# Optimization experiments

Hardware: AMD Instinct MI355X
Metric: run time of the kernel (lower is better)

## Reference

```python
import jax, jax.numpy as jnp
import numpy as np

N = 10000      # nodes
E = 160000     # edges
C = 128        # channels (hidden_irreps multiplicity)
NE = 10        # num_elements
G = 16         # num graphs
NB = 8         # num_bessel
RMAX = 5.0
PCUT = 5.0     # num_polynomial_cutoff
AVG_NN = 16.0
SQ3 = 3.0 ** 0.5


def _mlp(x, w1, w2, w3, wo):
    h = jax.nn.silu(x @ w1)
    h = jax.nn.silu(h @ w2)
    h = jax.nn.silu(h @ w3)
    return h @ wo


def _forward(positions, node_attrs, charges, shifts,
             W_emb, W_up1, Wr1_1, Wr1_2, Wr1_3, Wr1_o, Wlin1_s, Wlin1_v,
             P1_s1, P1_ss, P1_vv, P1_v1, P1_sv, Lp1_s, Lp1_v, R1,
             Wsk, Wup2_s, Wup2_v, Wr2_1, Wr2_2, Wr2_3, Wr2_o, Wlin2_s, Wlin2_v,
             P2_v1, P2_sv, Lp2_v, Rmid, Rout,
             edge_index, batch, num_graphs):
    snd, rcv = edge_index[0], edge_index[1]
    # edge vectors / lengths
    vec = positions[rcv] - positions[snd] + shifts                  # [E,3]
    length = jnp.sqrt(jnp.sum(vec * vec, -1) + 1e-12)               # [E]
    Yv = SQ3 * vec / length[:, None]                                # l=1 SH, component norm
    # Bessel radial basis * polynomial cutoff
    n = jnp.arange(1, NB + 1, dtype=positions.dtype)
    bess = (2.0 / RMAX) ** 0.5 * jnp.sin(n * jnp.pi * length[:, None] / RMAX) / length[:, None]
    u = length / RMAX
    p = PCUT
    fcut = jnp.where(u < 1.0,
                     1 - ((p + 1) * (p + 2) / 2) * u ** p + p * (p + 2) * u ** (p + 1)
                     - (p * (p + 1) / 2) * u ** (p + 2), 0.0)
    edge_feats = bess * fcut[:, None]                               # [E,NB]

    h = node_attrs @ W_emb                                          # node embedding [N,C]
    seg = lambda m: jax.ops.segment_sum(m, rcv, num_segments=N) / AVG_NN
    we = lambda Pm: node_attrs @ Pm                                 # element-dep. weights

    # ---- interaction / product / readout layer 1 (node feats are scalars) ----
    hu = h @ W_up1
    w = _mlp(edge_feats, Wr1_1, Wr1_2, Wr1_3, Wr1_o)                # [E,2C] TP weights
    w_ss, w_sv = w[:, :C], w[:, C:]
    hs_e = hu[snd]                                                  # gather sender feats
    A_s = seg(w_ss * hs_e)                                          # 0e x 0e -> 0e
    A_v = seg((w_sv * hs_e)[:, :, None] * Yv[:, None, :])           # 0e x 1o -> 1o
    A_s = A_s @ Wlin1_s
    A_v = jnp.einsum('ncd,ce->ned', A_v, Wlin1_v)
    # symmetric contraction (correlation=2), element-dependent weights
    B_s = we(P1_s1) * A_s + we(P1_ss) * A_s * A_s + we(P1_vv) * jnp.sum(A_v * A_v, -1) / SQ3
    B_v = we(P1_v1)[:, :, None] * A_v + we(P1_sv)[:, :, None] * A_s[:, :, None] * A_v
    h_s = B_s @ Lp1_s
    h_v = jnp.einsum('ncd,ce->ned', B_v, Lp1_v)
    dip1 = jnp.einsum('ncd,c->nd', h_v, R1)                         # linear dipole readout

    # ---- layer 2 (residual, output 128x1o) ----
    hs = h_s @ Wup2_s
    hv = jnp.einsum('ncd,ce->ned', h_v, Wup2_v)
    w2 = _mlp(edge_feats, Wr2_1, Wr2_2, Wr2_3, Wr2_o)               # [E,4C]
    w_a, w_b, w_c, w_d = w2[:, :C], w2[:, C:2 * C], w2[:, 2 * C:3 * C], w2[:, 3 * C:]
    hs_e, hv_e = hs[snd], hv[snd]
    m_s = w_a * hs_e + w_b * jnp.einsum('ecd,ed->ec', hv_e, Yv) / SQ3   # 0x0, 1x1->0
    m_v = (w_c * hs_e)[:, :, None] * Yv[:, None, :] + w_d[:, :, None] * hv_e  # 0x1,1x0->1
    A2_s = seg(m_s) @ Wlin2_s
    A2_v = jnp.einsum('ncd,ce->ned', seg(m_v), Wlin2_v)
    sc_v = jnp.einsum('ne,ecf,ncd->nfd', node_attrs, Wsk, h_v)      # skip TP (residual)
    B2_v = we(P2_v1)[:, :, None] * A2_v + we(P2_sv)[:, :, None] * A2_s[:, :, None] * A2_v
    h2_v = jnp.einsum('ncd,ce->ned', B2_v, Lp2_v) + sc_v
    # nonlinear dipole readout: input is pure 1o so gate scalars have no equivariant
    # path (zeros) -> sigmoid(0)=0.5 multiplier, as e3nn Gate would compute.
    mid = 0.5 * jnp.einsum('ncd,ck->nkd', h2_v, Rmid)               # [N,16,3]
    dip2 = jnp.einsum('nkd,k->nd', mid, Rout)

    atomic_dipoles = dip1 + dip2                                    # [N,3]
    total = jax.ops.segment_sum(atomic_dipoles, batch, num_segments=num_graphs)
    baseline = jax.ops.segment_sum(charges[:, None] * positions, batch, num_segments=num_graphs)
    return total + baseline, atomic_dipoles


def setup_inputs() -> dict:
    key = jax.random.key(0)
    ks = jax.random.split(key, 40)
    f32 = jnp.float32
    species = jax.random.randint(ks[0], (N,), 0, NE)
    w = lambda k, shape: jax.random.normal(k, shape, f32) / np.sqrt(shape[-2] if len(shape) > 1 else shape[0]).astype(np.float32)
    inp = dict(
        positions=jax.random.uniform(ks[1], (N, 3), f32) * 6.0,
        node_attrs=jax.nn.one_hot(species, NE, dtype=f32),
        charges=jax.random.normal(ks[2], (N,), f32),
        shifts=jnp.zeros((E, 3), f32),
        edge_index=jax.random.randint(ks[3], (2, E), 0, N),
        batch=jnp.sort(jax.random.randint(ks[4], (N,), 0, G)),
        ptr=jnp.arange(G + 1),
        W_emb=w(ks[5], (NE, C)), W_up1=w(ks[6], (C, C)),
        Wr1_1=w(ks[7], (NB, 64)), Wr1_2=w(ks[8], (64, 64)), Wr1_3=w(ks[9], (64, 64)),
        Wr1_o=w(ks[10], (64, 2 * C)), Wlin1_s=w(ks[11], (C, C)), Wlin1_v=w(ks[12], (C, C)),
        P1_s1=w(ks[13], (NE, C)), P1_ss=w(ks[14], (NE, C)), P1_vv=w(ks[15], (NE, C)),
        P1_v1=w(ks[16], (NE, C)), P1_sv=w(ks[17], (NE, C)),
        Lp1_s=w(ks[18], (C, C)), Lp1_v=w(ks[19], (C, C)),
        R1=jax.random.normal(ks[20], (C,), f32) / np.float32(np.sqrt(C)),
        Wsk=jax.random.normal(ks[21], (NE, C, C), f32) / np.float32(np.sqrt(C)),
        Wup2_s=w(ks[22], (C, C)), Wup2_v=w(ks[23], (C, C)),
        Wr2_1=w(ks[24], (NB, 64)), Wr2_2=w(ks[25], (64, 64)), Wr2_3=w(ks[26], (64, 64)),
        Wr2_o=w(ks[27], (64, 4 * C)), Wlin2_s=w(ks[28], (C, C)), Wlin2_v=w(ks[29], (C, C)),
        P2_v1=w(ks[30], (NE, C)), P2_sv=w(ks[31], (NE, C)), Lp2_v=w(ks[32], (C, C)),
        Rmid=w(ks[33], (C, 16)),
        Rout=jax.random.normal(ks[34], (16,), f32) / 4.0,
    )
    return inp


def reference(positions, node_attrs, charges, shifts, edge_index, batch, ptr,
              W_emb, W_up1, Wr1_1, Wr1_2, Wr1_3, Wr1_o, Wlin1_s, Wlin1_v,
              P1_s1, P1_ss, P1_vv, P1_v1, P1_sv, Lp1_s, Lp1_v, R1,
              Wsk, Wup2_s, Wup2_v, Wr2_1, Wr2_2, Wr2_3, Wr2_o, Wlin2_s, Wlin2_v,
              P2_v1, P2_sv, Lp2_v, Rmid, Rout):
    num_graphs = ptr.shape[0] - 1
    return _forward(positions, node_attrs, charges, shifts,
                    W_emb, W_up1, Wr1_1, Wr1_2, Wr1_3, Wr1_o, Wlin1_s, Wlin1_v,
                    P1_s1, P1_ss, P1_vv, P1_v1, P1_sv, Lp1_s, Lp1_v, R1,
                    Wsk, Wup2_s, Wup2_v, Wr2_1, Wr2_2, Wr2_3, Wr2_o, Wlin2_s, Wlin2_v,
                    P2_v1, P2_sv, Lp2_v, Rmid, Rout,
                    edge_index, batch, num_graphs)
```

## Files before the change

### kernel.cpp

```cpp
#include <hip/hip_runtime.h>

#define NN 10000
#define EE 160000
#define CC 128
#define NEL 10
#define NGR 16

static inline int cdiv(int a, int b) { return (a + b - 1) / b; }

__device__ __forceinline__ float silu_f(float x) { return x / (1.0f + __expf(-x)); }

__device__ __forceinline__ float bf2f(unsigned short u) {
    unsigned int x = ((unsigned int)u) << 16;
    return __uint_as_float(x);
}
__device__ __forceinline__ unsigned short f2bf(float f) {
    unsigned int x = __float_as_uint(f);
    unsigned int r = x + 0x7fffu + ((x >> 16) & 1u);
    return (unsigned short)(r >> 16);
}

typedef __attribute__((ext_vector_type(8))) short bf16x8;
typedef __attribute__((ext_vector_type(4))) float f32x4;

template <int KIN>
__global__ __launch_bounds__(256) void mfma_mlp3(
    const unsigned short* __restrict__ in,
    const unsigned short* __restrict__ W1t,
    const unsigned short* __restrict__ W2t,
    const unsigned short* __restrict__ W3t,
    unsigned short* __restrict__ out, int R)
{
    __shared__ __align__(16) unsigned short Ash[64 * KIN];
    __shared__ __align__(16) unsigned short W1s[64 * KIN];
    __shared__ __align__(16) unsigned short W2s[64 * 64];
    __shared__ __align__(16) unsigned short W3s[64 * 64];
    __shared__ __align__(16) unsigned short H1[64 * 64];
    __shared__ __align__(16) unsigned short H2[64 * 64];

    const int tid = threadIdx.x;
    const int w = tid >> 6;
    const int l = tid & 63;
    const int row0 = blockIdx.x * 64;

    constexpr int CPRa = KIN / 8;
    for (int cid = tid; cid < 64 * CPRa; cid += 256) {
        int r = cid / CPRa, k8 = cid % CPRa;
        int row = row0 + r;
        uint4 val = make_uint4(0u, 0u, 0u, 0u);
        if (row < R) val = *(const uint4*)(in + (size_t)row * KIN + k8 * 8);
        unsigned bo = ((unsigned)(r * KIN + k8 * 8) * 2u) ^ (((unsigned)(r & 7)) << 4);
        *(uint4*)((char*)Ash + bo) = val;
    }
    for (int cid = tid; cid < 64 * CPRa; cid += 256) {
        int nn = cid / CPRa, k8 = cid % CPRa;
        uint4 val = *(const uint4*)(W1t + (size_t)nn * KIN + k8 * 8);
        unsigned bo = ((unsigned)(nn * KIN + k8 * 8) * 2u) ^ (((unsigned)(nn & 7)) << 4);
        *(uint4*)((char*)W1s + bo) = val;
    }
    for (int cid = tid; cid < 64 * 8; cid += 256) {
        int nn = cid / 8, k8 = cid % 8;
        uint4 v2 = *(const uint4*)(W2t + (size_t)nn * 64 + k8 * 8);
        uint4 v3 = *(const uint4*)(W3t + (size_t)nn * 64 + k8 * 8);
        unsigned bo = ((unsigned)(nn * 64 + k8 * 8) * 2u) ^ (((unsigned)(nn & 7)) << 4);
        *(uint4*)((char*)W2s + bo) = v2;
        *(uint4*)((char*)W3s + bo) = v3;
    }
    __syncthreads();

    {
        f32x4 acc[4];
#pragma unroll
        for (int nt = 0; nt < 4; ++nt) acc[nt] = (f32x4){0.f, 0.f, 0.f, 0.f};
#pragma unroll
        for (int kc = 0; kc < KIN / 32; ++kc) {
            int r = w * 16 + (l & 15);
            int k = kc * 32 + (l >> 4) * 8;
            unsigned boA = ((unsigned)(r * KIN + k) * 2u) ^ (((unsigned)(r & 7)) << 4);
            bf16x8 afr = *(const bf16x8*)((char*)Ash + boA);
#pragma unroll
            for (int nt = 0; nt < 4; ++nt) {
                int col = nt * 16 + (l & 15);
                unsigned boB = ((unsigned)(col * KIN + k) * 2u) ^ (((unsigned)(col & 7)) << 4);
                bf16x8 bfr = *(const bf16x8*)((char*)W1s + boB);
                acc[nt] = __builtin_amdgcn_mfma_f32_16x16x32_bf16(afr, bfr, acc[nt], 0, 0, 0);
            }
        }
#pragma unroll
        for (int nt = 0; nt < 4; ++nt)
#pragma unroll
            for (int rg = 0; rg < 4; ++rg) {
                int row = w * 16 + (l >> 4) * 4 + rg;
                int col = nt * 16 + (l & 15);
                unsigned bo = ((unsigned)(row * 64 + col) * 2u) ^ (((unsigned)(row & 7)) << 4);
                *(unsigned short*)((char*)H1 + bo) = f2bf(silu_f(acc[nt][rg]));
            }
    }
    __syncthreads();

    {
        f32x4 acc[4];
#pragma unroll
        for (int nt = 0; nt < 4; ++nt) acc[nt] = (f32x4){0.f, 0.f, 0.f, 0.f};
#pragma unroll
        for (int kc = 0; kc < 2; ++kc) {
            int r = w * 16 + (l & 15);
            int k = kc * 32 + (l >> 4) * 8;
            unsigned boA = ((unsigned)(r * 64 + k) * 2u) ^ (((unsigned)(r & 7)) << 4);
            bf16x8 afr = *(const bf16x8*)((char*)H1 + boA);
#pragma unroll
            for (int nt = 0; nt < 4; ++nt) {
                int col = nt * 16 + (l & 15);
                unsigned boB = ((unsigned)(col * 64 + k) * 2u) ^ (((unsigned)(col & 7)) << 4);
                bf16x8 bfr = *(const bf16x8*)((char*)W2s + boB);
                acc[nt] = __builtin_amdgcn_mfma_f32_16x16x32_bf16(afr, bfr, acc[nt], 0, 0, 0);
            }
        }
#pragma unroll
        for (int nt = 0; nt < 4; ++nt)
#pragma unroll
            for (int rg = 0; rg < 4; ++rg) {
                int row = w * 16 + (l >> 4) * 4 + rg;
                int col = nt * 16 + (l & 15);
                unsigned bo = ((unsigned)(row * 64 + col) * 2u) ^ (((unsigned)(row & 7)) << 4);
                *(unsigned short*)((char*)H2 + bo) = f2bf(silu_f(acc[nt][rg]));
            }
    }
    __syncthreads();

    {
        f32x4 acc[4];
#pragma unroll
        for (int nt = 0; nt < 4; ++nt) acc[nt] = (f32x4){0.f, 0.f, 0.f, 0.f};
#pragma unroll
        for (int kc = 0; kc < 2; ++kc) {
            int r = w * 16 + (l & 15);
            int k = kc * 32 + (l >> 4) * 8;
            unsigned boA = ((unsigned)(r * 64 + k) * 2u) ^ (((unsigned)(r & 7)) << 4);
            bf16x8 afr = *(const bf16x8*)((char*)H2 + boA);
#pragma unroll
            for (int nt = 0; nt < 4; ++nt) {
                int col = nt * 16 + (l & 15);
                unsigned boB = ((unsigned)(col * 64 + k) * 2u) ^ (((unsigned)(col & 7)) << 4);
                bf16x8 bfr = *(const bf16x8*)((char*)W3s + boB);
                acc[nt] = __builtin_amdgcn_mfma_f32_16x16x32_bf16(afr, bfr, acc[nt], 0, 0, 0);
            }
        }
#pragma unroll
        for (int nt = 0; nt < 4; ++nt)
#pragma unroll
            for (int rg = 0; rg < 4; ++rg) {
                int row = row0 + w * 16 + (l >> 4) * 4 + rg;
                if (row < R) {
                    int col = nt * 16 + (l & 15);
                    out[(size_t)row * 64 + col] = f2bf(silu_f(acc[nt][rg]));
                }
            }
    }
}

template <int K, int N, int MODE>
__global__ __launch_bounds__(256) void mfma_gemm(
    const unsigned short* __restrict__ in, int in_ld,
    const unsigned short* __restrict__ Wt,
    unsigned short* __restrict__ out, int out_ld,
    int R)
{
    constexpr int NT = N / 16;
    constexpr int KC = K / 32;
    constexpr int CPR = K / 8;
    __shared__ __align__(16) unsigned short Ash[64 * K];
    __shared__ __align__(16) unsigned short Bsh[N * K];

    const int tid = threadIdx.x;
    const int w = tid >> 6;
    const int l = tid & 63;
    const int row0 = blockIdx.x * 64;
    const int cb = blockIdx.y * N;

    for (int cid = tid; cid < 64 * CPR; cid += 256) {
        int r = cid / CPR, k8 = cid % CPR;
        int row = row0 + r;
        uint4 val = make_uint4(0u, 0u, 0u, 0u);
        if (row < R) val = *(const uint4*)(in + (size_t)row * in_ld + k8 * 8);
        unsigned bo = ((unsigned)(r * K + k8 * 8) * 2u) ^ (((unsigned)(r & 7)) << 4);
        *(uint4*)((char*)Ash + bo) = val;
    }
    for (int cid = tid; cid < N * CPR; cid += 256) {
        int nn = cid / CPR, k8 = cid % CPR;
        uint4 val = *(const uint4*)(Wt + (size_t)(cb + nn) * K + k8 * 8);
        unsigned bo = ((unsigned)(nn * K + k8 * 8) * 2u) ^ (((unsigned)(nn & 7)) << 4);
        *(uint4*)((char*)Bsh + bo) = val;
    }
    __syncthreads();

    bf16x8 afr[KC];
#pragma unroll
    for (int kc = 0; kc < KC; ++kc) {
        int r = w * 16 + (l & 15);
        int k = kc * 32 + (l >> 4) * 8;
        unsigned bo = ((unsigned)(r * K + k) * 2u) ^ (((unsigned)(r & 7)) << 4);
        afr[kc] = *(const bf16x8*)((char*)Ash + bo);
    }

    f32x4 acc[NT];
#pragma unroll
    for (int nt = 0; nt < NT; ++nt) {
        acc[nt] = (f32x4){0.f, 0.f, 0.f, 0.f};
#pragma unroll
        for (int kc = 0; kc < KC; ++kc) {
            int col = nt * 16 + (l & 15);
            int k = kc * 32 + (l >> 4) * 8;
            unsigned bo = ((unsigned)(col * K + k) * 2u) ^ (((unsigned)(col & 7)) << 4);
            bf16x8 bfr = *(const bf16x8*)((char*)Bsh + bo);
            acc[nt] = __builtin_amdgcn_mfma_f32_16x16x32_bf16(afr[kc], bfr, acc[nt], 0, 0, 0);
        }
    }

#pragma unroll
    for (int nt = 0; nt < NT; ++nt) {
#pragma unroll
        for (int rg = 0; rg < 4; ++rg) {
            int row = row0 + w * 16 + (l >> 4) * 4 + rg;
            if (row < R) {
                int col = cb + nt * 16 + (l & 15);
                float v = acc[nt][rg];
                if constexpr (MODE == 1) v = silu_f(v);
                out[(size_t)row * out_ld + col] = f2bf(v);
            }
        }
    }
}

template <int K, int N, int MODE>
__global__ __launch_bounds__(256) void mfma_gemm_f32(
    const float* __restrict__ in, int in_ld,
    const unsigned short* __restrict__ Wt,
    float* __restrict__ out, int out_ld,
    int R, float scale)
{
    constexpr int NT = N / 16;
    constexpr int KC = K / 32;
    constexpr int CPR = K / 8;
    __shared__ __align__(16) unsigned short Ash[64 * K];
    __shared__ __align__(16) unsigned short Bsh[N * K];

    const int tid = threadIdx.x;
    const int w = tid >> 6;
    const int l = tid & 63;
    const int row0 = blockIdx.x * 64;
    const int cb = blockIdx.y * N;

    for (int cid = tid; cid < 64 * CPR; cid += 256) {
        int r = cid / CPR, k8 = cid % CPR;
        int row = row0 + r;
        union { unsigned short u16[8]; uint4 v; } pk;
        if (row < R) {
            const float* p = in + (size_t)row * in_ld + k8 * 8;
            float4 f0 = *(const float4*)p;
            float4 f1 = *(const float4*)(p + 4);
            pk.u16[0] = f2bf(f0.x); pk.u16[1] = f2bf(f0.y);
            pk.u16[2] = f2bf(f0.z); pk.u16[3] = f2bf(f0.w);
            pk.u16[4] = f2bf(f1.x); pk.u16[5] = f2bf(f1.y);
            pk.u16[6] = f2bf(f1.z); pk.u16[7] = f2bf(f1.w);
        } else {
            pk.v = make_uint4(0u, 0u, 0u, 0u);
        }
        unsigned bo = ((unsigned)(r * K + k8 * 8) * 2u) ^ (((unsigned)(r & 7)) << 4);
        *(uint4*)((char*)Ash + bo) = pk.v;
    }
    for (int cid = tid; cid < N * CPR; cid += 256) {
        int nn = cid / CPR, k8 = cid % CPR;
        uint4 val = *(const uint4*)(Wt + (size_t)(cb + nn) * K + k8 * 8);
        unsigned bo = ((unsigned)(nn * K + k8 * 8) * 2u) ^ (((unsigned)(nn & 7)) << 4);
        *(uint4*)((char*)Bsh + bo) = val;
    }
    __syncthreads();

    bf16x8 afr[KC];
#pragma unroll
    for (int kc = 0; kc < KC; ++kc) {
        int r = w * 16 + (l & 15);
        int k = kc * 32 + (l >> 4) * 8;
        unsigned bo = ((unsigned)(r * K + k) * 2u) ^ (((unsigned)(r & 7)) << 4);
        afr[kc] = *(const bf16x8*)((char*)Ash + bo);
    }

    f32x4 acc[NT];
#pragma unroll
    for (int nt = 0; nt < NT; ++nt) {
        acc[nt] = (f32x4){0.f, 0.f, 0.f, 0.f};
#pragma unroll
        for (int kc = 0; kc < KC; ++kc) {
            int col = nt * 16 + (l & 15);
            int k = kc * 32 + (l >> 4) * 8;
            unsigned bo = ((unsigned)(col * K + k) * 2u) ^ (((unsigned)(col & 7)) << 4);
            bf16x8 bfr = *(const bf16x8*)((char*)Bsh + bo);
            acc[nt] = __builtin_amdgcn_mfma_f32_16x16x32_bf16(afr[kc], bfr, acc[nt], 0, 0, 0);
        }
    }

#pragma unroll
    for (int nt = 0; nt < NT; ++nt) {
#pragma unroll
        for (int rg = 0; rg < 4; ++rg) {
            int row = row0 + w * 16 + (l >> 4) * 4 + rg;
            if (row < R) {
                int col = cb + nt * 16 + (l & 15);
                float v = acc[nt][rg] * scale;
                size_t idx = (size_t)row * out_ld + col;
                if constexpr (MODE == 6)      out[idx] += v;
                else if constexpr (MODE == 2) ((unsigned short*)out)[idx] = f2bf(v);
                else                          out[idx] = v;
            }
        }
    }
}

struct WPE { const float* s[8]; unsigned short* d[8]; int K[8], N[8], Kp[8]; };
__global__ void k_wprepE(WPE wp)
{
    int m = blockIdx.y;
    int i = blockIdx.x * 256 + threadIdx.x;
    int tot = wp.N[m] * wp.Kp[m];
    if (i >= tot) return;
    int n = i / wp.Kp[m], k = i % wp.Kp[m];
    wp.d[m][i] = (k < wp.K[m]) ? f2bf(wp.s[m][k * wp.N[m] + n]) : (unsigned short)0;
}

struct WP10 { const float* s[10]; unsigned short* d[10]; };
__global__ void k_wprep10(WP10 wp)
{
    int m = blockIdx.y;
    int i = blockIdx.x * 256 + threadIdx.x;
    if (i >= 128 * 128) return;
    int n = i / 128, k = i % 128;
    wp.d[m][i] = f2bf(wp.s[m][k * 128 + n]);
}

__global__ void k_count(const int* __restrict__ rcv, int* __restrict__ deg)
{
    int e = blockIdx.x * 256 + threadIdx.x;
    if (e < EE) atomicAdd(&deg[rcv[e]], 1);
}

__global__ __launch_bounds__(256) void k_scan(const int* __restrict__ deg,
                                              int* __restrict__ rowptr,
                                              int* __restrict__ cursor)
{
    __shared__ int part[256];
    const int t = threadIdx.x;
    const int PER = (NN + 255) / 256;
    int base = t * PER;
    int s = 0;
    for (int j = 0; j < PER; ++j) { int idx = base + j; if (idx < NN) s += deg[idx]; }
    part[t] = s;
    __syncthreads();
    for (int off = 1; off < 256; off <<= 1) {
        int v = (t >= off) ? part[t - off] : 0;
        __syncthreads();
        part[t] += v;
        __syncthreads();
    }
    int run = (t == 0) ? 0 : part[t - 1];
    for (int j = 0; j < PER; ++j) {
        int idx = base + j;
        if (idx < NN) { rowptr[idx] = run; cursor[idx] = run; run += deg[idx]; }
    }
    if (t == 255) rowptr[NN] = part[255];
}

__global__ void k_fill(const int* __restrict__ rcv, int* __restrict__ cursor,
                       int* __restrict__ perm)
{
    int e = blockIdx.x * 256 + threadIdx.x;
    if (e >= EE) return;
    int pos = atomicAdd(&cursor[rcv[e]], 1);
    perm[pos] = e;
}

__global__ __launch_bounds__(256) void k_sortwave(const int* __restrict__ rowptr,
                                                  int* __restrict__ perm)
{
    int gid = blockIdx.x * 256 + threadIdx.x;
    int wid = gid >> 6;
    int lane = gid & 63;
    if (wid >= NN) return;
    int a = rowptr[wid], b = rowptr[wid + 1];
    int d = b - a;
    if (d <= 1) return;
    if (d <= 64) {
        int v = (lane < d) ? perm[a + lane] : 0x7fffffff;
        int rank = 0;
        for (int j = 0; j < 64; ++j) {
            int vj = __shfl(v, j);
            if (j < d && vj < v) ++rank;
        }
        if (lane < d) perm[a + rank] = v;
    } else if (lane == 0) {
        for (int i = a + 1; i < b; ++i) {
            int v = perm[i]; int j = i - 1;
            while (j >= a && perm[j] > v) { perm[j + 1] = perm[j]; --j; }
            perm[j + 1] = v;
        }
    }
}

__global__ void k_geom_perm(const float* __restrict__ pos, const float* __restrict__ shifts,
                            const int* __restrict__ snd, const int* __restrict__ rcv,
                            const int* __restrict__ perm,
                            float* __restrict__ Yv, unsigned short* __restrict__ efb,
                            int* __restrict__ psnd)
{
    int i = blockIdx.x * 256 + threadIdx.x;
    if (i >= EE) return;
    int e = perm[i];
    int s = snd[e], r = rcv[e];
    psnd[i] = s;
    float vx = pos[r * 3 + 0] - pos[s * 3 + 0] + shifts[e * 3 + 0];
    float vy = pos[r * 3 + 1] - pos[s * 3 + 1] + shifts[e * 3 + 1];
    float vz = pos[r * 3 + 2] - pos[s * 3 + 2] + shifts[e * 3 + 2];
    float len = sqrtf(vx * vx + vy * vy + vz * vz + 1e-12f);
    float inv = 1.0f / len;
    const float SQ3 = 1.7320508075688772f;
    Yv[i * 3 + 0] = SQ3 * vx * inv;
    Yv[i * 3 + 1] = SQ3 * vy * inv;
    Yv[i * 3 + 2] = SQ3 * vz * inv;
    float u = len * 0.2f;
    float fc = 0.0f;
    if (u < 1.0f) {
        float u2 = u * u, u4 = u2 * u2, u5 = u4 * u, u6 = u5 * u, u7 = u6 * u;
        fc = 1.0f - 21.0f * u5 + 35.0f * u6 - 15.0f * u7;
    }
    float pref = 0.6324555320336759f * inv * fc;
    const float PIO5 = 0.6283185307179586f;
    union { unsigned short u16[8]; uint4 v; } pk;
#pragma unroll
    for (int n = 1; n <= 8; ++n)
        pk.u16[n - 1] = f2bf(pref * sinf((float)n * PIO5 * len));
    uint4* dst = (uint4*)(efb + (size_t)i * 32);
    dst[0] = pk.v;
    dst[1] = make_uint4(0u, 0u, 0u, 0u);
    dst[2] = make_uint4(0u, 0u, 0u, 0u);
    dst[3] = make_uint4(0u, 0u, 0u, 0u);
}

__global__ __launch_bounds__(256) void k_gather1(
    const int* __restrict__ rowptr, const int* __restrict__ psnd,
    const float* __restrict__ Yv, const unsigned short* __restrict__ wb,
    int e0, int e1,
    const unsigned short* __restrict__ gS,
    float* __restrict__ outS, float* __restrict__ outV)
{
    const int t = threadIdx.x;
    const int c = t & 127;
    const int n = blockIdx.x * 2 + (t >> 7);
    if (n >= NN) return;
    int rs = rowptr[n], re = rowptr[n + 1];
    if (rs < e0) rs = e0;
    if (re > e1) re = e1;
    if (rs >= re) return;
    float accs = 0.f, a0 = 0.f, a1 = 0.f, a2 = 0.f;
    for (int i = rs; i < re; ++i) {
        const unsigned short* wp = wb + (size_t)(i - e0) * 256;
        float wss = bf2f(wp[c]);
        float wsv = bf2f(wp[128 + c]);
        float h = bf2f(gS[psnd[i] * 128 + c]);
        float y0 = Yv[i * 3], y1 = Yv[i * 3 + 1], y2 = Yv[i * 3 + 2];
        accs = fmaf(wss, h, accs);
        float tv = wsv * h;
        a0 = fmaf(tv, y0, a0); a1 = fmaf(tv, y1, a1); a2 = fmaf(tv, y2, a2);
    }
    outS[n * 128 + c] += accs;
    outV[n * 384 + c]       += a0;
    outV[n * 384 + 128 + c] += a1;
    outV[n * 384 + 256 + c] += a2;
}

__global__ __launch_bounds__(256) void k_gather23(
    const int* __restrict__ rowptr, const int* __restrict__ psnd,
    const float* __restrict__ Yv, const unsigned short* __restrict__ wb,
    int e0, int e1,
    const unsigned short* __restrict__ gS, const unsigned short* __restrict__ gV,
    float* __restrict__ outS, float* __restrict__ outV)
{
    const int t = threadIdx.x;
    const int c = t & 127;
    const int n = blockIdx.x * 2 + (t >> 7);
    if (n >= NN) return;
    int rs = rowptr[n], re = rowptr[n + 1];
    if (rs < e0) rs = e0;
    if (re > e1) re = e1;
    if (rs >= re) return;
    float accs = 0.f, a0 = 0.f, a1 = 0.f, a2 = 0.f;
    for (int i = rs; i < re; ++i) {
        const unsigned short* wp = wb + (size_t)(i - e0) * 512;
        float wa = bf2f(wp[c]);
        float wbv = bf2f(wp[128 + c]);
        float wc = bf2f(wp[256 + c]);
        float wd = bf2f(wp[384 + c]);
        int s = psnd[i];
        float hs = bf2f(gS[s * 128 + c]);
        float v0 = bf2f(gV[s * 384 + c]);
        float v1 = bf2f(gV[s * 384 + 128 + c]);
        float v2 = bf2f(gV[s * 384 + 256 + c]);
        float y0 = Yv[i * 3], y1 = Yv[i * 3 + 1], y2 = Yv[i * 3 + 2];
        float hd = v0 * y0 + v1 * y1 + v2 * y2;
        accs = fmaf(wa, hs, accs);
        accs = fmaf(wbv, hd * 0.57735026919f, accs);
        float tv = wc * hs;
        a0 = fmaf(tv, y0, a0); a0 = fmaf(wd, v0, a0);
        a1 = fmaf(tv, y1, a1); a1 = fmaf(wd, v1, a1);
        a2 = fmaf(tv, y2, a2); a2 = fmaf(wd, v2, a2);
    }
    outS[n * 128 + c] += accs;
    outV[n * 384 + c]       += a0;
    outV[n * 384 + 128 + c] += a1;
    outV[n * 384 + 256 + c] += a2;
}

__global__ void k_embed2(const float* __restrict__ attrs, const float* __restrict__ W_emb,
                         int* __restrict__ species, float* __restrict__ h)
{
    int t = blockIdx.x * 256 + threadIdx.x;
    if (t >= NN * CC) return;
    int n = t >> 7, c = t & 127;
    int sp = 0;
#pragma unroll
    for (int j = 0; j < NEL; ++j)
        if (attrs[n * NEL + j] > 0.5f) sp = j;
    if (c == 0) species[n] = sp;
    h[t] = W_emb[sp * CC + c];
}

__global__ void k_B1(const int* __restrict__ species,
                     const float* __restrict__ As_l, const float* __restrict__ Av_l,
                     const float* __restrict__ P_s1, const float* __restrict__ P_ss,
                     const float* __restrict__ P_vv, const float* __restrict__ P_v1,
                     const float* __restrict__ P_sv,
                     float* __restrict__ Bs, float* __restrict__ Bv)
{
    int t = blockIdx.x * 256 + threadIdx.x;
    if (t >= NN * CC) return;
    int n = t >> 7, c = t & 127;
    int sp = species[n];
    int pb = sp * CC + c;
    int vb = n * 384 + c;
    float as = As_l[t];
    float a0 = Av_l[vb], a1 = Av_l[vb + CC], a2 = Av_l[vb + 2 * CC];
    Bs[t] = P_s1[pb] * as + P_ss[pb] * as * as
          + P_vv[pb] * (a0 * a0 + a1 * a1 + a2 * a2) * 0.57735026919f;
    float tv = P_v1[pb] + P_sv[pb] * as;
    Bv[vb] = tv * a0; Bv[vb + CC] = tv * a1; Bv[vb + 2 * CC] = tv * a2;
}

__global__ void k_B2(const int* __restrict__ species,
                     const float* __restrict__ As_l, const float* __restrict__ Av_l,
                     const float* __restrict__ P_v1, const float* __restrict__ P_sv,
                     float* __restrict__ Bv)
{
    int t = blockIdx.x * 256 + threadIdx.x;
    if (t >= NN * CC) return;
    int n = t >> 7, c = t & 127;
    int sp = species[n];
    int pb = sp * CC + c;
    int vb = n * 384 + c;
    float as = As_l[t];
    float tv = P_v1[pb] + P_sv[pb] * as;
    Bv[vb] = tv * Av_l[vb];
    Bv[vb + CC] = tv * Av_l[vb + CC];
    Bv[vb + 2 * CC] = tv * Av_l[vb + 2 * CC];
}

__global__ void k_sc(const int* __restrict__ species, const float* __restrict__ h_v,
                     const float* __restrict__ Wsk, float* __restrict__ h2v)
{
    int n = blockIdx.x, f = threadIdx.x;
    int sp = species[n];
    const float* Wp = Wsk + sp * (CC * CC);
    const float* hvn = h_v + n * 384;
    float a0 = 0.f, a1 = 0.f, a2 = 0.f;
    for (int c = 0; c < CC; ++c) {
        float w = Wp[c * CC + f];
        a0 = fmaf(hvn[c], w, a0);
        a1 = fmaf(hvn[CC + c], w, a1);
        a2 = fmaf(hvn[2 * CC + c], w, a2);
    }
    h2v[n * 384 + f] = a0;
    h2v[n * 384 + CC + f] = a1;
    h2v[n * 384 + 2 * CC + f] = a2;
}

__global__ void k_node_out2(const float* __restrict__ h2v, const float* __restrict__ h_v,
                            const float* __restrict__ R1,
                            const float* __restrict__ Rmid, const float* __restrict__ Rout,
                            const float* __restrict__ charges, const float* __restrict__ pos,
                            float* __restrict__ out, float* __restrict__ tot)
{
    int n = blockIdx.x, l = threadIdx.x;
    float r0 = 0.f, r1 = 0.f;
#pragma unroll
    for (int k = 0; k < 16; ++k) {
        r0 = fmaf(Rmid[l * 16 + k], Rout[k], r0);
        r1 = fmaf(Rmid[(64 + l) * 16 + k], Rout[k], r1);
    }
    const float* hb = h2v + n * 384;
    const float* hv1 = h_v + n * 384;
    float R1a = R1[l], R1b = R1[64 + l];
    float red[3];
#pragma unroll
    for (int d = 0; d < 3; ++d) {
        float v = hb[d * CC + l] * r0 + hb[d * CC + 64 + l] * r1;
        float dv = hv1[d * CC + l] * R1a + hv1[d * CC + 64 + l] * R1b;
        float m = dv + 0.5f * v;
        for (int o = 32; o > 0; o >>= 1) m += __shfl_down(m, o);
        red[d] = m;
    }
    if (l == 0) {
        float q = charges[n];
#pragma unroll
        for (int d = 0; d < 3; ++d) {
            float a = red[d];
            out[48 + n * 3 + d] = a;
            tot[n * 3 + d] = a + q * pos[n * 3 + d];
        }
    }
}

__global__ __launch_bounds__(256) void k_greduce(const float* __restrict__ tot,
                                                 const int* __restrict__ batch,
                                                 float* __restrict__ out)
{
    __shared__ float r[256 * 3];
    const int g = blockIdx.x;
    const int t = threadIdx.x;
    float s0 = 0.f, s1 = 0.f, s2 = 0.f;
    for (int n = t; n < NN; n += 256) {
        if (batch[n] == g) {
            s0 += tot[n * 3]; s1 += tot[n * 3 + 1]; s2 += tot[n * 3 + 2];
        }
    }
    r[t] = s0; r[256 + t] = s1; r[512 + t] = s2;
    __syncthreads();
    for (int off = 128; off > 0; off >>= 1) {
        if (t < off) {
            r[t] += r[t + off];
            r[256 + t] += r[256 + t + off];
            r[512 + t] += r[512 + t + off];
        }
        __syncthreads();
    }
    if (t < 3) out[g * 3 + t] = r[t * 256];
}

extern "C" void kernel_launch(void* const* d_in, const int* in_sizes, int n_in,
                              void* d_out, int out_size, void* d_ws, size_t ws_size,
                              hipStream_t stream)
{
    const float* positions = (const float*)d_in[0];
    const float* node_attrs = (const float*)d_in[1];
    const float* charges = (const float*)d_in[2];
    const float* shifts = (const float*)d_in[3];
    const int*   eidx = (const int*)d_in[4];
    const int*   batch = (const int*)d_in[5];
    const float* W_emb  = (const float*)d_in[7];
    const float* W_up1  = (const float*)d_in[8];
    const float* Wr1_1  = (const float*)d_in[9];
    const float* Wr1_2  = (const float*)d_in[10];
    const float* Wr1_3  = (const float*)d_in[11];
    const float* Wr1_o  = (const float*)d_in[12];
    const float* Wlin1_s = (const float*)d_in[13];
    const float* Wlin1_v = (const float*)d_in[14];
    const float* P1_s1 = (const float*)d_in[15];
    const float* P1_ss = (const float*)d_in[16];
    const float* P1_vv = (const float*)d_in[17];
    const float* P1_v1 = (const float*)d_in[18];
    const float* P1_sv = (const float*)d_in[19];
    const float* Lp1_s = (const float*)d_in[20];
    const float* Lp1_v = (const float*)d_in[21];
    const float* R1    = (const float*)d_in[22];
    const float* Wsk   = (const float*)d_in[23];
    const float* Wup2_s = (const float*)d_in[24];
    const float* Wup2_v = (const float*)d_in[25];
    const float* Wr2_1 = (const float*)d_in[26];
    const float* Wr2_2 = (const float*)d_in[27];
    const float* Wr2_3 = (const float*)d_in[28];
    const float* Wr2_o = (const float*)d_in[29];
    const float* Wlin2_s = (const float*)d_in[30];
    const float* Wlin2_v = (const float*)d_in[31];
    const float* P2_v1 = (const float*)d_in[32];
    const float* P2_sv = (const float*)d_in[33];
    const float* Lp2_v = (const float*)d_in[34];
    const float* Rmid  = (const float*)d_in[35];
    const float* Rout  = (const float*)d_in[36];
    (void)in_sizes; (void)n_in; (void)out_size;

    const int* snd = eidx;
    const int* rcv = eidx + EE;
    float* out = (float*)d_out;

    char* ws = (char*)d_ws;
    size_t off = 0;
    auto alloc = [&](size_t bytes) -> void* {
        void* p = (void*)(ws + off);
        off = (off + bytes + 255) & ~(size_t)255;
        return p;
    };
    int*   species = (int*)alloc((size_t)NN * 4);
    int*   deg     = (int*)alloc((size_t)NN * 4);
    int*   rowptr  = (int*)alloc((size_t)(NN + 16) * 4);
    int*   cursor  = (int*)alloc((size_t)NN * 4);
    int*   perm    = (int*)alloc((size_t)EE * 4);
    int*   psnd    = (int*)alloc((size_t)EE * 4);
    float* Yv   = (float*)alloc((size_t)EE * 3 * 4);
    unsigned short* efb = (unsigned short*)alloc((size_t)EE * 32 * 2);
    float* A_s  = (float*)alloc((size_t)NN * CC * 4);
    float* A_v  = (float*)alloc((size_t)NN * 3 * CC * 4);
    float* hbuf = (float*)alloc((size_t)NN * CC * 4);
    float* hu   = (float*)alloc((size_t)NN * CC * 4);
    float* h_v  = (float*)alloc((size_t)NN * 3 * CC * 4);
    float* h2v  = (float*)alloc((size_t)NN * 3 * CC * 4);
    float* tot  = (float*)alloc((size_t)NN * 3 * 4);
    unsigned short* hub = (unsigned short*)alloc((size_t)NN * CC * 2);
    unsigned short* hsb = (unsigned short*)alloc((size_t)NN * CC * 2);
    unsigned short* hvb = (unsigned short*)alloc((size_t)NN * 3 * CC * 2);
    unsigned short* W1t_l1 = (unsigned short*)alloc(64 * 32 * 2);
    unsigned short* W2t_l1 = (unsigned short*)alloc(64 * 64 * 2);
    unsigned short* W3t_l1 = (unsigned short*)alloc(64 * 64 * 2);
    unsigned short* Wot_l1 = (unsigned short*)alloc(256 * 64 * 2);
    unsigned short* W1t_l2 = (unsigned short*)alloc(64 * 32 * 2);
    unsigned short* W2t_l2 = (unsigned short*)alloc(64 * 64 * 2);
    unsigned short* W3t_l2 = (unsigned short*)alloc(64 * 64 * 2);
    unsigned short* Wot_l2 = (unsigned short*)alloc(512 * 64 * 2);
    unsigned short* Wn[10];
    for (int m = 0; m < 10; ++m) Wn[m] = (unsigned short*)alloc(128 * 128 * 2);
    unsigned short* hbA = (unsigned short*)alloc((size_t)EE * 64 * 2);

    int C = 16;
    if      (off + (size_t)EE * 512 * 2 + 4096 <= ws_size)        C = 1;
    else if (off + (size_t)(EE / 2) * 512 * 2 + 4096 <= ws_size)  C = 2;
    else if (off + (size_t)(EE / 4) * 512 * 2 + 4096 <= ws_size)  C = 4;
    else if (off + (size_t)(EE / 8) * 512 * 2 + 4096 <= ws_size)  C = 8;
    const int EC = EE / C;
    unsigned short* wbuf = (unsigned short*)alloc((size_t)EC * 512 * 2);

    const float inv16 = 1.0f / 16.0f;
    const float one = 1.0f;

    hipMemsetAsync(deg, 0, (size_t)NN * 4, stream);
    hipMemsetAsync(A_s, 0, (size_t)NN * 4 * CC * 4, stream);

    {
        WPE wp;
        const float* s[8] = {Wr1_1, Wr1_2, Wr1_3, Wr1_o, Wr2_1, Wr2_2, Wr2_3, Wr2_o};
        unsigned short* d[8] = {W1t_l1, W2t_l1, W3t_l1, Wot_l1, W1t_l2, W2t_l2, W3t_l2, Wot_l2};
        int Ks[8] = {8, 64, 64, 64, 8, 64, 64, 64};
        int Ns[8] = {64, 64, 64, 256, 64, 64, 64, 512};
        int Kp[8] = {32, 64, 64, 64, 32, 64, 64, 64};
        for (int m = 0; m < 8; ++m) { wp.s[m] = s[m]; wp.d[m] = d[m]; wp.K[m] = Ks[m]; wp.N[m] = Ns[m]; wp.Kp[m] = Kp[m]; }
        k_wprepE<<<dim3(cdiv(512 * 64, 256), 8), 256, 0, stream>>>(wp);
    }
    {
        WP10 wp;
        const float* srcs[10] = {W_up1, Wlin1_s, Wlin1_v, Lp1_s, Lp1_v,
                                 Wup2_s, Wup2_v, Wlin2_s, Wlin2_v, Lp2_v};
        for (int m = 0; m < 10; ++m) { wp.s[m] = srcs[m]; wp.d[m] = Wn[m]; }
        k_wprep10<<<dim3(cdiv(128 * 128, 256), 10), 256, 0, stream>>>(wp);
    }

    k_count<<<cdiv(EE, 256), 256, 0, stream>>>(rcv, deg);
    k_scan<<<1, 256, 0, stream>>>(deg, rowptr, cursor);
    k_fill<<<cdiv(EE, 256), 256, 0, stream>>>(rcv, cursor, perm);
    k_sortwave<<<cdiv(NN * 64, 256), 256, 0, stream>>>(rowptr, perm);
    k_geom_perm<<<cdiv(EE, 256), 256, 0, stream>>>(positions, shifts, snd, rcv, perm, Yv, efb, psnd);

    k_embed2<<<cdiv(NN * CC, 256), 256, 0, stream>>>(node_attrs, W_emb, species, hbuf);

    mfma_gemm_f32<128, 128, 2><<<cdiv(NN, 64), 256, 0, stream>>>(
        hbuf, 128, Wn[0], (float*)hub, 128, NN, one);

    mfma_mlp3<32><<<cdiv(EE, 64), 256, 0, stream>>>(efb, W1t_l1, W2t_l1, W3t_l1, hbA, EE);
    for (int ch = 0; ch < C; ++ch) {
        int e0 = ch * EC, e1 = e0 + EC;
        mfma_gemm<64, 128, 2><<<dim3(cdiv(EC, 64), 2), 256, 0, stream>>>(
            hbA + (size_t)e0 * 64, 64, Wot_l1, wbuf, 256, EC);
        k_gather1<<<NN / 2, 256, 0, stream>>>(
            rowptr, psnd, Yv, wbuf, e0, e1, hub, A_s, A_v);
    }

    mfma_gemm_f32<128, 128, 0><<<cdiv(NN, 64), 256, 0, stream>>>(
        A_s, 128, Wn[1], A_s, 128, NN, inv16);
    mfma_gemm_f32<128, 128, 0><<<cdiv(3 * NN, 64), 256, 0, stream>>>(
        A_v, 128, Wn[2], A_v, 128, 3 * NN, inv16);
    k_B1<<<cdiv(NN * CC, 256), 256, 0, stream>>>(
        species, A_s, A_v, P1_s1, P1_ss, P1_vv, P1_v1, P1_sv, hbuf , A_v );
    mfma_gemm_f32<128, 128, 0><<<cdiv(NN, 64), 256, 0, stream>>>(
        hbuf, 128, Wn[3], hu , 128, NN, one);
    mfma_gemm_f32<128, 128, 0><<<cdiv(3 * NN, 64), 256, 0, stream>>>(
        A_v , 128, Wn[4], h_v, 128, 3 * NN, one);
    mfma_gemm_f32<128, 128, 2><<<cdiv(NN, 64), 256, 0, stream>>>(
        hu , 128, Wn[5], (float*)hsb, 128, NN, one);
    mfma_gemm_f32<128, 128, 2><<<cdiv(3 * NN, 64), 256, 0, stream>>>(
        h_v, 128, Wn[6], (float*)hvb, 128, 3 * NN, one);

    hipMemsetAsync(A_s, 0, (size_t)NN * 4 * CC * 4, stream);
    mfma_mlp3<32><<<cdiv(EE, 64), 256, 0, stream>>>(efb, W1t_l2, W2t_l2, W3t_l2, hbA, EE);
    for (int ch = 0; ch < C; ++ch) {
        int e0 = ch * EC, e1 = e0 + EC;
        mfma_gemm<64, 128, 2><<<dim3(cdiv(EC, 64), 4), 256, 0, stream>>>(
            hbA + (size_t)e0 * 64, 64, Wot_l2, wbuf, 512, EC);
        k_gather23<<<NN / 2, 256, 0, stream>>>(
            rowptr, psnd, Yv, wbuf, e0, e1, hsb, hvb, A_s, A_v);
    }

    mfma_gemm_f32<128, 128, 0><<<cdiv(NN, 64), 256, 0, stream>>>(
        A_s, 128, Wn[7], A_s, 128, NN, inv16);
    mfma_gemm_f32<128, 128, 0><<<cdiv(3 * NN, 64), 256, 0, stream>>>(
        A_v, 128, Wn[8], A_v, 128, 3 * NN, inv16);
    k_sc<<<NN, 128, 0, stream>>>(species, h_v, Wsk, h2v);
    k_B2<<<cdiv(NN * CC, 256), 256, 0, stream>>>(species, A_s, A_v, P2_v1, P2_sv, A_v );
    mfma_gemm_f32<128, 128, 6><<<cdiv(3 * NN, 64), 256, 0, stream>>>(
        A_v , 128, Wn[9], h2v, 128, 3 * NN, one);

    k_node_out2<<<NN, 64, 0, stream>>>(h2v, h_v, R1, Rmid, Rout, charges, positions, out, tot);
    k_greduce<<<NGR, 256, 0, stream>>>(tot, batch, out);
}
```

Before: 500.2 us.

## Fuse per-node sort with edge geometry and precompute species-projected embedding table

```diff
diff --git a/kernel.cpp b/kernel.cpp
--- a/kernel.cpp
+++ b/kernel.cpp
@@ -338,6 +338,33 @@
     wp.d[m][i] = f2bf(wp.s[m][k * 128 + n]);
 }
 
+__global__ void k_emb2mm(const float* __restrict__ W_emb, const float* __restrict__ W_up1,
+                         unsigned short* __restrict__ EMB2)
+{
+    int i = blockIdx.x * 256 + threadIdx.x;
+    if (i >= NEL * CC) return;
+    int s = i / CC, c = i % CC;
+    float acc = 0.f;
+    for (int k = 0; k < CC; ++k)
+        acc = fmaf(W_emb[s * CC + k], W_up1[k * CC + c], acc);
+    EMB2[i] = f2bf(acc);
+}
+
+__global__ void k_spec_hub(const float* __restrict__ attrs,
+                           const unsigned short* __restrict__ EMB2,
+                           int* __restrict__ species, unsigned short* __restrict__ hub)
+{
+    int t = blockIdx.x * 256 + threadIdx.x;
+    if (t >= NN * CC) return;
+    int n = t >> 7, c = t & 127;
+    int sp = 0;
+#pragma unroll
+    for (int j = 0; j < NEL; ++j)
+        if (attrs[n * NEL + j] > 0.5f) sp = j;
+    if (c == 0) species[n] = sp;
+    hub[t] = EMB2[sp * CC + c];
+}
+
 __global__ void k_count(const int* __restrict__ rcv, int* __restrict__ deg)
 {
     int e = blockIdx.x * 256 + threadIdx.x;
@@ -379,42 +406,12 @@
     perm[pos] = e;
 }
 
-__global__ __launch_bounds__(256) void k_sortwave(const int* __restrict__ rowptr,
-                                                  int* __restrict__ perm)
-{
-    int gid = blockIdx.x * 256 + threadIdx.x;
-    int wid = gid >> 6;
-    int lane = gid & 63;
-    if (wid >= NN) return;
-    int a = rowptr[wid], b = rowptr[wid + 1];
-    int d = b - a;
-    if (d <= 1) return;
-    if (d <= 64) {
-        int v = (lane < d) ? perm[a + lane] : 0x7fffffff;
-        int rank = 0;
-        for (int j = 0; j < 64; ++j) {
-            int vj = __shfl(v, j);
-            if (j < d && vj < v) ++rank;
-        }
-        if (lane < d) perm[a + rank] = v;
-    } else if (lane == 0) {
-        for (int i = a + 1; i < b; ++i) {
-            int v = perm[i]; int j = i - 1;
-            while (j >= a && perm[j] > v) { perm[j + 1] = perm[j]; --j; }
-            perm[j + 1] = v;
-        }
-    }
-}
-
-__global__ void k_geom_perm(const float* __restrict__ pos, const float* __restrict__ shifts,
-                            const int* __restrict__ snd, const int* __restrict__ rcv,
-                            const int* __restrict__ perm,
-                            float* __restrict__ Yv, unsigned short* __restrict__ efb,
-                            int* __restrict__ psnd)
-{
-    int i = blockIdx.x * 256 + threadIdx.x;
-    if (i >= EE) return;
-    int e = perm[i];
+__device__ __forceinline__ void geom_one(
+    const float* __restrict__ pos, const float* __restrict__ shifts,
+    const int* __restrict__ snd, const int* __restrict__ rcv,
+    int e, int i, float* __restrict__ Yv, unsigned short* __restrict__ efb,
+    int* __restrict__ psnd)
+{
     int s = snd[e], r = rcv[e];
     psnd[i] = s;
     float vx = pos[r * 3 + 0] - pos[s * 3 + 0] + shifts[e * 3 + 0];
@@ -443,6 +440,43 @@
     dst[1] = make_uint4(0u, 0u, 0u, 0u);
     dst[2] = make_uint4(0u, 0u, 0u, 0u);
     dst[3] = make_uint4(0u, 0u, 0u, 0u);
+}
+
+__global__ __launch_bounds__(256) void k_sortgeom(
+    const int* __restrict__ rowptr, int* __restrict__ perm,
+    const float* __restrict__ pos, const float* __restrict__ shifts,
+    const int* __restrict__ snd, const int* __restrict__ rcv,
+    float* __restrict__ Yv, unsigned short* __restrict__ efb,
+    int* __restrict__ psnd)
+{
+    int gid = blockIdx.x * 256 + threadIdx.x;
+    int wid = gid >> 6;
+    int lane = gid & 63;
+    if (wid >= NN) return;
+    int a = rowptr[wid], b = rowptr[wid + 1];
+    int d = b - a;
+    if (d <= 0) return;
+    if (d <= 64) {
+        int v = (lane < d) ? perm[a + lane] : 0x7fffffff;
+        int rank = 0;
+        for (int j = 0; j < 64; ++j) {
+            int vj = __shfl(v, j);
+            if (j < d && vj < v) ++rank;
+        }
+        if (lane < d)
+            geom_one(pos, shifts, snd, rcv, v, a + rank, Yv, efb, psnd);
+    } else {
+        if (lane == 0) {
+            for (int i = a + 1; i < b; ++i) {
+                int v = perm[i]; int j = i - 1;
+                while (j >= a && perm[j] > v) { perm[j + 1] = perm[j]; --j; }
+                perm[j + 1] = v;
+            }
+            __threadfence();
+        }
+        for (int i = a + lane; i < b; i += 64)
+            geom_one(pos, shifts, snd, rcv, perm[i], i, Yv, efb, psnd);
+    }
 }
 
 __global__ __launch_bounds__(256) void k_gather1(
@@ -517,20 +551,6 @@
     outV[n * 384 + c]       += a0;
     outV[n * 384 + 128 + c] += a1;
     outV[n * 384 + 256 + c] += a2;
-}
-
-__global__ void k_embed2(const float* __restrict__ attrs, const float* __restrict__ W_emb,
-                         int* __restrict__ species, float* __restrict__ h)
-{
-    int t = blockIdx.x * 256 + threadIdx.x;
-    if (t >= NN * CC) return;
-    int n = t >> 7, c = t & 127;
-    int sp = 0;
-#pragma unroll
-    for (int j = 0; j < NEL; ++j)
-        if (attrs[n * NEL + j] > 0.5f) sp = j;
-    if (c == 0) species[n] = sp;
-    h[t] = W_emb[sp * CC + c];
 }
 
 __global__ void k_B1(const int* __restrict__ species,
@@ -724,6 +744,7 @@
     unsigned short* hub = (unsigned short*)alloc((size_t)NN * CC * 2);
     unsigned short* hsb = (unsigned short*)alloc((size_t)NN * CC * 2);
     unsigned short* hvb = (unsigned short*)alloc((size_t)NN * 3 * CC * 2);
+    unsigned short* EMB2 = (unsigned short*)alloc(NEL * CC * 2);
     unsigned short* W1t_l1 = (unsigned short*)alloc(64 * 32 * 2);
     unsigned short* W2t_l1 = (unsigned short*)alloc(64 * 64 * 2);
     unsigned short* W3t_l1 = (unsigned short*)alloc(64 * 64 * 2);
@@ -767,17 +788,15 @@
         for (int m = 0; m < 10; ++m) { wp.s[m] = srcs[m]; wp.d[m] = Wn[m]; }
         k_wprep10<<<dim3(cdiv(128 * 128, 256), 10), 256, 0, stream>>>(wp);
     }
+    k_emb2mm<<<cdiv(NEL * CC, 256), 256, 0, stream>>>(W_emb, W_up1, EMB2);
 
     k_count<<<cdiv(EE, 256), 256, 0, stream>>>(rcv, deg);
     k_scan<<<1, 256, 0, stream>>>(deg, rowptr, cursor);
     k_fill<<<cdiv(EE, 256), 256, 0, stream>>>(rcv, cursor, perm);
-    k_sortwave<<<cdiv(NN * 64, 256), 256, 0, stream>>>(rowptr, perm);
-    k_geom_perm<<<cdiv(EE, 256), 256, 0, stream>>>(positions, shifts, snd, rcv, perm, Yv, efb, psnd);
-
-    k_embed2<<<cdiv(NN * CC, 256), 256, 0, stream>>>(node_attrs, W_emb, species, hbuf);
-
-    mfma_gemm_f32<128, 128, 2><<<cdiv(NN, 64), 256, 0, stream>>>(
-        hbuf, 128, Wn[0], (float*)hub, 128, NN, one);
+    k_sortgeom<<<cdiv(NN * 64, 256), 256, 0, stream>>>(
+        rowptr, perm, positions, shifts, snd, rcv, Yv, efb, psnd);
+
+    k_spec_hub<<<cdiv(NN * CC, 256), 256, 0, stream>>>(node_attrs, EMB2, species, hub);
 
     mfma_mlp3<32><<<cdiv(EE, 64), 256, 0, stream>>>(efb, W1t_l1, W2t_l1, W3t_l1, hbA, EE);
     for (int ch = 0; ch < C; ++ch) {
```

New measurement: 493.9 us. Within noise of the previous version (-1.3%).
